# Optimization experiments

Hardware: AMD Instinct MI355X
Metric: run time of the kernel (lower is better)

The kernel has to match this reference:

```python
import jax, jax.numpy as jnp
import numpy as np

B, T, D, FF, H, K = 8, 1024, 512, 2048, 8, 15
HD = D // H  # key_dim = d_model // num_heads


def _ln(x, g, b):
    # keras LayerNormalization default epsilon = 1e-3
    m = jnp.mean(x, axis=-1, keepdims=True)
    v = jnp.var(x, axis=-1, keepdims=True)
    return (x - m) * jax.lax.rsqrt(v + 1e-3) * g + b


def setup_inputs() -> dict:
    key = jax.random.key(0)
    ks = iter(jax.random.split(key, 64))

    def rn(shape, s=0.02):
        return jax.random.normal(next(ks), shape, jnp.float32) * s

    p = {}
    p['x'] = jax.random.normal(next(ks), (B, T, D), jnp.float32)
    # ff_pre: LN -> Dense(FF, relu) -> Dense(D)
    p['g1'] = jnp.ones((D,), jnp.float32); p['b1'] = jnp.zeros((D,), jnp.float32)
    p['Wff1'] = rn((D, FF)); p['bff1'] = jnp.zeros((FF,), jnp.float32)
    p['Wff2'] = rn((FF, D)); p['bff2'] = jnp.zeros((D,), jnp.float32)
    # attention norm + MHA projections (keras EinsumDense shapes)
    p['ga'] = jnp.ones((D,), jnp.float32); p['ba'] = jnp.zeros((D,), jnp.float32)
    p['Wq'] = rn((D, H, HD)); p['bq'] = jnp.zeros((H, HD), jnp.float32)
    p['Wk'] = rn((D, H, HD)); p['bk'] = jnp.zeros((H, HD), jnp.float32)
    p['Wv'] = rn((D, H, HD)); p['bv'] = jnp.zeros((H, HD), jnp.float32)
    p['Wo'] = rn((H, HD, D)); p['bo'] = jnp.zeros((D,), jnp.float32)
    # conv branch: LN -> pointwise conv (2D, gelu) -> depthwise conv(k=15) -> BN -> swish -> pointwise conv (D)
    p['gc'] = jnp.ones((D,), jnp.float32); p['bc'] = jnp.zeros((D,), jnp.float32)
    p['Wcp'] = rn((D, 2 * D)); p['bcp'] = jnp.zeros((2 * D,), jnp.float32)
    p['dwk'] = rn((K, 1, 2 * D)); p['dwb'] = jnp.zeros((2 * D,), jnp.float32)
    p['bn_g'] = jnp.ones((2 * D,), jnp.float32); p['bn_b'] = jnp.zeros((2 * D,), jnp.float32)
    p['bn_m'] = jnp.zeros((2 * D,), jnp.float32)
    p['bn_v'] = jnp.ones((2 * D,), jnp.float32)
    p['Wco'] = rn((2 * D, D)); p['bco'] = jnp.zeros((D,), jnp.float32)
    # ff_post
    p['g2'] = jnp.ones((D,), jnp.float32); p['b2'] = jnp.zeros((D,), jnp.float32)
    p['Wf1'] = rn((D, FF)); p['bf1'] = jnp.zeros((FF,), jnp.float32)
    p['Wf2'] = rn((FF, D)); p['bf2'] = jnp.zeros((D,), jnp.float32)
    return p


def reference(x, g1, b1, Wff1, bff1, Wff2, bff2, ga, ba, Wq, bq, Wk, bk, Wv, bv, Wo, bo, gc, bc, Wcp, bcp, dwk, dwb, bn_g, bn_b, bn_m, bn_v, Wco, bco, g2, b2, Wf1, bf1, Wf2, bf2):
    # Macaron FFN (pre), half-step residual applied later
    x_ff = jnp.maximum(_ln(x, g1, b1) @ Wff1 + bff1, 0.0) @ Wff2 + bff2

    # causal multi-head self-attention (cache=None path)
    a = _ln(x, ga, ba)
    q = jnp.einsum('btd,dhk->bthk', a, Wq) + bq
    k = jnp.einsum('btd,dhk->bthk', a, Wk) + bk
    v = jnp.einsum('btd,dhk->bthk', a, Wv) + bv
    scores = jnp.einsum('bqhd,bkhd->bhqk', q, k) / jnp.sqrt(jnp.float32(HD))
    causal = jnp.tril(jnp.ones((T, T), bool))  # [T,T]
    scores = jnp.where(causal, scores, jnp.float32(-1e9))
    w = jax.nn.softmax(scores, axis=-1)
    ctx = jnp.einsum('bhqk,bkhd->bqhd', w, v)
    attn = jnp.einsum('bqhd,hdo->bqo', ctx, Wo) + bo

    x = x + 0.5 * x_ff + attn

    # convolution module: pointwise(gelu) -> causal left-pad -> depthwise -> BN(inference) -> swish -> pointwise
    c = jax.nn.gelu(_ln(x, gc, bc) @ Wcp + bcp, approximate=False)
    c = jnp.pad(c, ((0, 0), (K - 1, 0), (0, 0)))  # causal pad
    c = jax.lax.conv_general_dilated(
        c, dwk, window_strides=(1,), padding='VALID',
        dimension_numbers=('NWC', 'WIO', 'NWC'), feature_group_count=2 * D) + dwb
    c = (c - bn_m) * jax.lax.rsqrt(bn_v + 1e-3) * bn_g + bn_b
    c = c * jax.nn.sigmoid(c)  # swish
    c = c @ Wco + bco
    x = x + c

    # post FFN (full residual)
    x = x + (jnp.maximum(_ln(x, g2, b2) @ Wf1 + bf1, 0.0) @ Wf2 + bf2)
    return x
```

## Files before the change

### kernel.cpp

```cpp
#include <hip/hip_runtime.h>
#include <hip/hip_bf16.h>
#include <math.h>

#define BB 8
#define TT 1024
#define DD 512
#define FFD 2048
#define HH 8
#define HDD 64
#define KW 15
#define MR (BB*TT)
#define QKVN 1536

typedef __attribute__((ext_vector_type(8))) short short8;
typedef __attribute__((ext_vector_type(4))) short short4v;
typedef __attribute__((ext_vector_type(4))) float f32x4;
typedef __hip_bfloat16 bf16;

__device__ __forceinline__ float bf2f(unsigned u16) {
    return __uint_as_float(u16 << 16);
}

__device__ __forceinline__ void async_copy16(const void* g, void* l) {
    __builtin_amdgcn_global_load_lds(
        (const __attribute__((address_space(1))) void*)g,
        (__attribute__((address_space(3))) void*)l, 16, 0, 0);
}

__device__ __forceinline__ float gelu_exact(float v) {
    return 0.5f * v * (1.0f + erff(v * 0.70710678118654752f));
}

struct PrepPack {
    const float* src[10];
    bf16*        dst[10];
    int          K[10];
    int          lgNT[10];
    float        scale[10];
    int          off[10];
    const float* bq; const float* bk; const float* bv;
    float*       bdst;
    const float* x;
    const float* g1; const float* b1; const float* ga; const float* ba;
    bf16* o1; bf16* o2;
};

__global__ __launch_bounds__(256) void prep_kernel(PrepPack P) {
    __shared__ alignas(16) bf16 T[64][72];
    const int bid = blockIdx.x;
    if (bid == 1536) {
        #pragma unroll
        for (int it = 0; it < 6; ++it) {
            int i = it * 256 + threadIdx.x;
            float v = i < 512 ? P.bq[i] * 0.125f
                              : (i < 1024 ? P.bk[i - 512] : P.bv[i - 1024]);
            P.bdst[i] = v;
        }
        return;
    }
    if (bid > 1536) {
        int wave = ((bid - 1537) * 256 + (int)threadIdx.x) >> 6;
        int lane = threadIdx.x & 63;
        const float* row = P.x + (size_t)wave * DD;
        float4 v0 = ((const float4*)row)[lane];
        float4 v1 = ((const float4*)row)[64 + lane];
        float s  = v0.x + v0.y + v0.z + v0.w + v1.x + v1.y + v1.z + v1.w;
        float ss = v0.x*v0.x + v0.y*v0.y + v0.z*v0.z + v0.w*v0.w
                 + v1.x*v1.x + v1.y*v1.y + v1.z*v1.z + v1.w*v1.w;
        #pragma unroll
        for (int off = 32; off >= 1; off >>= 1) {
            s  += __shfl_xor(s,  off, 64);
            ss += __shfl_xor(ss, off, 64);
        }
        float mean = s * (1.0f / DD);
        float var  = ss * (1.0f / DD) - mean * mean;
        float r    = rsqrtf(var + 1e-3f);
        float n0x = (v0.x - mean) * r, n0y = (v0.y - mean) * r,
              n0z = (v0.z - mean) * r, n0w = (v0.w - mean) * r;
        float n1x = (v1.x - mean) * r, n1y = (v1.y - mean) * r,
              n1z = (v1.z - mean) * r, n1w = (v1.w - mean) * r;
        {
            float4 g0 = ((const float4*)P.g1)[lane];
            float4 gg = ((const float4*)P.g1)[64 + lane];
            float4 b0 = ((const float4*)P.b1)[lane];
            float4 bb = ((const float4*)P.b1)[64 + lane];
            alignas(8) bf16 o0[4], o1[4];
            o0[0] = __float2bfloat16(n0x * g0.x + b0.x);
            o0[1] = __float2bfloat16(n0y * g0.y + b0.y);
            o0[2] = __float2bfloat16(n0z * g0.z + b0.z);
            o0[3] = __float2bfloat16(n0w * g0.w + b0.w);
            o1[0] = __float2bfloat16(n1x * gg.x + bb.x);
            o1[1] = __float2bfloat16(n1y * gg.y + bb.y);
            o1[2] = __float2bfloat16(n1z * gg.z + bb.z);
            o1[3] = __float2bfloat16(n1w * gg.w + bb.w);
            bf16* orow = P.o1 + (size_t)wave * DD;
            *(short4v*)(orow + lane * 4)       = *(const short4v*)o0;
            *(short4v*)(orow + 256 + lane * 4) = *(const short4v*)o1;
        }
        {
            float4 g0 = ((const float4*)P.ga)[lane];
            float4 gg = ((const float4*)P.ga)[64 + lane];
            float4 b0 = ((const float4*)P.ba)[lane];
            float4 bb = ((const float4*)P.ba)[64 + lane];
            alignas(8) bf16 o0[4], o1[4];
            o0[0] = __float2bfloat16(n0x * g0.x + b0.x);
            o0[1] = __float2bfloat16(n0y * g0.y + b0.y);
            o0[2] = __float2bfloat16(n0z * g0.z + b0.z);
            o0[3] = __float2bfloat16(n0w * g0.w + b0.w);
            o1[0] = __float2bfloat16(n1x * gg.x + bb.x);
            o1[1] = __float2bfloat16(n1y * gg.y + bb.y);
            o1[2] = __float2bfloat16(n1z * gg.z + bb.z);
            o1[3] = __float2bfloat16(n1w * gg.w + bb.w);
            bf16* orow = P.o2 + (size_t)wave * DD;
            *(short4v*)(orow + lane * 4)       = *(const short4v*)o0;
            *(short4v*)(orow + 256 + lane * 4) = *(const short4v*)o1;
        }
        return;
    }
    int e = 0;
    #pragma unroll
    for (int i = 1; i < 10; ++i) e = (bid >= P.off[i]) ? i : e;
    const float* W  = P.src[e];
    bf16*        Wt = P.dst[e];
    const int    K  = P.K[e];
    const int    lg = P.lgNT[e];
    const float  scale = P.scale[e];
    const int local = bid - P.off[e];
    const int bx = local & ((1 << lg) - 1);
    const int by = local >> lg;
    const int k0 = by * 64;
    const int n0 = bx * 64;
    const int N  = (1 << lg) * 64;
    const int tid = threadIdx.x;
    #pragma unroll
    for (int it = 0; it < 4; ++it) {
        int lin = it * 256 + tid;
        int kl  = lin >> 4;
        int nq  = (lin & 15) * 4;
        float4 v = *(const float4*)(W + (size_t)(k0 + kl) * N + n0 + nq);
        T[nq + 0][kl] = __float2bfloat16(v.x * scale);
        T[nq + 1][kl] = __float2bfloat16(v.y * scale);
        T[nq + 2][kl] = __float2bfloat16(v.z * scale);
        T[nq + 3][kl] = __float2bfloat16(v.w * scale);
    }
    __syncthreads();
    #pragma unroll
    for (int it = 0; it < 4; ++it) {
        int lin = it * 256 + tid;
        int nl  = lin >> 4;
        int kq  = (lin & 15) * 4;
        *(short4v*)(Wt + (size_t)(n0 + nl) * K + k0 + kq) = *(const short4v*)&T[nl][kq];
    }
}

template<int BN, int OP, int RESMODE, int OUTMODE>
__global__ __launch_bounds__(256) void bgemm_kernel(
    const bf16* __restrict__ A,
    const bf16* __restrict__ Bt,
    const float* __restrict__ bias,
    const float* __restrict__ res1,
    const bf16* __restrict__ res2,
    float s2, float oscale,
    void* __restrict__ Cout,
    int N, int Kd, int nxb)
{
    constexpr int NT = BN / 32;
    constexpr int S  = 4 + BN / 32;
    __shared__ alignas(16) bf16 As[2][128][64];
    __shared__ alignas(16) bf16 Bs[2][BN][64];
    const int tid  = threadIdx.x;
    const int w    = tid >> 6;
    const int lane = tid & 63;
    const int quad = lane >> 4;
    const int l16  = lane & 15;
    const int wm   = w >> 1, wn = w & 1;

    const int flat = blockIdx.x;
    const int c8   = flat & 7;
    const int j    = flat >> 3;
    const int jy   = j / nxb;
    const int m0   = (c8 * 8 + jy) * 128;
    const int n0   = (j - jy * nxb) * BN;

    const int srow = lane >> 3;
    const int scol = ((lane & 7) ^ srow) * 8;

    const bf16* Ap = A  + (size_t)(m0 + w * 32 + srow) * Kd + scol;
    const bf16* Bp = Bt + (size_t)(n0 + w * (BN / 4) + srow) * Kd + scol;

    f32x4 acc[4][NT] = {};
    const int nk = Kd >> 6;

#define BSTAGE(bb, kk) do { \
        _Pragma("unroll") \
        for (int i = 0; i < 4; ++i) \
            async_copy16(Ap + (size_t)(i * 8) * Kd + (kk), &As[bb][w * 32 + i * 8][0]); \
        _Pragma("unroll") \
        for (int i = 0; i < BN / 32; ++i) \
            async_copy16(Bp + (size_t)(i * 8) * Kd + (kk), &Bs[bb][w * (BN / 4) + i * 8][0]); \
    } while (0)

    BSTAGE(0, 0);
    for (int t = 0; t < nk; ++t) {
        const int cur = t & 1;
        if (t + 1 < nk) {
            BSTAGE(cur ^ 1, (t + 1) * 64);
            if constexpr (S == 6) asm volatile("s_waitcnt vmcnt(6)" ::: "memory");
            else                  asm volatile("s_waitcnt vmcnt(8)" ::: "memory");
        } else {
            asm volatile("s_waitcnt vmcnt(0)" ::: "memory");
        }
        __builtin_amdgcn_s_barrier();
        __builtin_amdgcn_sched_barrier(0);
        __builtin_amdgcn_s_setprio(1);
        #pragma unroll
        for (int ks = 0; ks < 2; ++ks) {
            short8 af[4], bfr[NT];
            #pragma unroll
            for (int mt = 0; mt < 4; ++mt) {
                const int row = wm * 64 + mt * 16 + l16;
                const int c   = ((ks * 4 + quad) ^ (row & 7)) * 16;
                af[mt] = *(const short8*)((const char*)&As[cur][row][0] + c);
            }
            #pragma unroll
            for (int nt = 0; nt < NT; ++nt) {
                const int col = wn * (BN / 2) + nt * 16 + l16;
                const int c   = ((ks * 4 + quad) ^ (col & 7)) * 16;
                bfr[nt] = *(const short8*)((const char*)&Bs[cur][col][0] + c);
            }
            #pragma unroll
            for (int mt = 0; mt < 4; ++mt)
                #pragma unroll
                for (int nt = 0; nt < NT; ++nt)
                    acc[mt][nt] = __builtin_amdgcn_mfma_f32_16x16x32_bf16(
                        af[mt], bfr[nt], acc[mt][nt], 0, 0, 0);
        }
        __builtin_amdgcn_s_setprio(0);
        asm volatile("" ::: "memory");
        __builtin_amdgcn_s_barrier();
    }
#undef BSTAGE

    const int crow0 = m0 + wm * 64 + quad * 4;
    const int ccol0 = n0 + wn * (BN / 2) + l16;
    #pragma unroll
    for (int nt = 0; nt < NT; ++nt) {
        const int col = ccol0 + nt * 16;
        const float bv = bias[col];
        #pragma unroll
        for (int mt = 0; mt < 4; ++mt) {
            #pragma unroll
            for (int r = 0; r < 4; ++r) {
                const int row = crow0 + mt * 16 + r;
                const size_t off = (size_t)row * N + col;
                float o = acc[mt][nt][r] + bv;
                if (OP == 1)      o = fmaxf(o, 0.f);
                else if (OP == 2) o = gelu_exact(o);
                if (RESMODE >= 1) o += res1[off];
                if (RESMODE == 2) o += s2 * __bfloat162float(res2[off]);
                if (OUTMODE == 0) ((float*)Cout)[off] = o;
                else              ((bf16*)Cout)[off]  = __float2bfloat16(o * oscale);
            }
        }
    }
}

template<int NK, int RESMODE>
__global__ __launch_bounds__(512, 1) void fusedln_kernel(
    const bf16* __restrict__ A, const bf16* __restrict__ Bt,
    const float* __restrict__ bias,
    const float* __restrict__ res1, const bf16* __restrict__ res2, float s2,
    float* __restrict__ outF,
    const float* __restrict__ g, const float* __restrict__ bb,
    bf16* __restrict__ lnout)
{
    constexpr int Kd = NK * 64;
    __shared__ alignas(16) char lds[2 * 69632];
    const int tid  = threadIdx.x;
    const int w    = tid >> 6;
    const int lane = tid & 63;
    const int quad = lane >> 4;
    const int l16  = lane & 15;
    const int wm   = w >> 2, wn = w & 3;
    const int m0   = (int)blockIdx.x * 32;

    const int srow = lane >> 3;
    const int swz  = ((lane & 7) ^ srow) * 8;
    const bf16* BpS = Bt + (size_t)(w * 64 + srow) * Kd + swz;
    const bf16* ApS = A  + (size_t)(m0 + (w & 3) * 8 + srow) * Kd + swz;

#define FSTG(kc, base) do { \
        _Pragma("unroll") \
        for (int i = 0; i < 8; ++i) \
            async_copy16(BpS + (size_t)(i * 8) * Kd + (kc), \
                         lds + (base) + (w * 64 + i * 8) * 128); \
        if (w < 4) \
            async_copy16(ApS + (kc), \
                         lds + (base) + 65536 + ((w & 3) * 8) * 128); \
    } while (0)

    const int cxa0 = ((quad)     ^ (l16 & 7)) * 16;
    const int cxa1 = ((4 + quad) ^ (l16 & 7)) * 16;

    f32x4 acc[8] = {};

    FSTG(0, 0);
    for (int t = 0; t < NK; ++t) {
        const int cb = (t & 1) * 69632;
        if (t + 1 < NK) {
            FSTG((t + 1) * 64, ((t + 1) & 1) * 69632);
            asm volatile("s_waitcnt vmcnt(8)" ::: "memory");
        } else {
            asm volatile("s_waitcnt vmcnt(0)" ::: "memory");
        }
        __builtin_amdgcn_s_barrier();
        __builtin_amdgcn_sched_barrier(0);
        __builtin_amdgcn_s_setprio(1);

        const char* abase = lds + cb + 65536 + (wm * 16 + l16) * 128;
        short8 a0 = *(const short8*)(abase + cxa0);
        short8 a1 = *(const short8*)(abase + cxa1);
        #pragma unroll
        for (int nt = 0; nt < 8; ++nt) {
            const char* bbase = lds + cb + (wn * 128 + nt * 16 + l16) * 128;
            short8 b0 = *(const short8*)(bbase + cxa0);
            short8 b1 = *(const short8*)(bbase + cxa1);
            acc[nt] = __builtin_amdgcn_mfma_f32_16x16x32_bf16(a0, b0, acc[nt], 0, 0, 0);
            acc[nt] = __builtin_amdgcn_mfma_f32_16x16x32_bf16(a1, b1, acc[nt], 0, 0, 0);
        }
        __builtin_amdgcn_s_setprio(0);
        asm volatile("" ::: "memory");
        __builtin_amdgcn_s_barrier();
    }
#undef FSTG

    const int row0 = m0 + wm * 16 + quad * 4;
    float val[8][4];
    float s[4] = {0.f, 0.f, 0.f, 0.f}, ss[4] = {0.f, 0.f, 0.f, 0.f};
    #pragma unroll
    for (int nt = 0; nt < 8; ++nt) {
        const int col = wn * 128 + nt * 16 + l16;
        const float bv = bias[col];
        #pragma unroll
        for (int r = 0; r < 4; ++r) {
            const size_t off = (size_t)(row0 + r) * DD + col;
            float o = acc[nt][r] + bv;
            if (RESMODE >= 1) o += res1[off];
            if (RESMODE == 2) o += s2 * __bfloat162float(res2[off]);
            outF[off] = o;
            val[nt][r] = o;
            s[r]  += o;
            ss[r] += o * o;
        }
    }
    #pragma unroll
    for (int off = 8; off >= 1; off >>= 1) {
        #pragma unroll
        for (int r = 0; r < 4; ++r) {
            s[r]  += __shfl_xor(s[r],  off, 64);
            ss[r] += __shfl_xor(ss[r], off, 64);
        }
    }
    __syncthreads();
    float2* red = (float2*)lds;
    if (l16 == 0) {
        #pragma unroll
        for (int r = 0; r < 4; ++r) {
            float2 v; v.x = s[r]; v.y = ss[r];
            red[wn * 32 + (wm * 16 + quad * 4 + r)] = v;
        }
    }
    __syncthreads();
    float mean[4], rstd[4];
    #pragma unroll
    for (int r = 0; r < 4; ++r) {
        float a = 0.f, b2 = 0.f;
        #pragma unroll
        for (int q = 0; q < 4; ++q) {
            float2 v = red[q * 32 + (wm * 16 + quad * 4 + r)];
            a += v.x; b2 += v.y;
        }
        const float m = a * (1.0f / DD);
        const float var = b2 * (1.0f / DD) - m * m;
        mean[r] = m;
        rstd[r] = rsqrtf(var + 1e-3f);
    }
    #pragma unroll
    for (int nt = 0; nt < 8; ++nt) {
        const int col = wn * 128 + nt * 16 + l16;
        const float gv = g[col], bv2 = bb[col];
        #pragma unroll
        for (int r = 0; r < 4; ++r) {
            const size_t off = (size_t)(row0 + r) * DD + col;
            lnout[off] = __float2bfloat16(
                (val[nt][r] - mean[r]) * rstd[r] * gv + bv2);
        }
    }
}

__global__ __launch_bounds__(512, 2) void gemm256_kernel(
    const bf16* __restrict__ Aff, const bf16* __restrict__ Btff,
    const float* __restrict__ biasff, bf16* __restrict__ outff,
    const bf16* __restrict__ Aqk, const bf16* __restrict__ Btqk,
    const float* __restrict__ biasqk, bf16* __restrict__ qkvb,
    bf16* __restrict__ Vtb, int nffblk)
{
    __shared__ alignas(16) char lds[131072];
    const int tid  = threadIdx.x;
    const int w    = tid >> 6;
    const int lane = tid & 63;
    const int quad = lane >> 4;
    const int l16  = lane & 15;
    const int ms   = w >> 2, ns = w & 3;

    const bool jobq = (int)blockIdx.x >= nffblk;
    const int  flat = jobq ? (int)blockIdx.x - nffblk : (int)blockIdx.x;
    const int  nxb  = jobq ? 6 : 8;
    const bf16* A   = jobq ? Aqk : Aff;
    const bf16* Bt  = jobq ? Btqk : Btff;
    const float* bias = jobq ? biasqk : biasff;

    const int c8 = flat & 7;
    const int j  = flat >> 3;
    const int jy = j / nxb;
    const int m0 = (c8 * 4 + jy) * 256;
    const int n0 = (j - jy * nxb) * 256;

    const int srow = lane >> 3;
    const int swz  = ((lane & 7) ^ srow) * 8;
    const bf16* ApS = A  + (size_t)(m0 + w * 16 + srow) * DD + swz;
    const bf16* BpS = Bt + (size_t)(n0 + w * 16 + srow) * DD + swz;

#define STG_A(half, kc, nbase) do { \
        async_copy16(ApS + (size_t)((half) * 128) * DD + (kc), \
                     lds + (nbase) + (half) * 16384 + (w * 16) * 128); \
        async_copy16(ApS + (size_t)((half) * 128 + 8) * DD + (kc), \
                     lds + (nbase) + (half) * 16384 + (w * 16 + 8) * 128); \
    } while (0)
#define STG_B(half, kc, nbase) do { \
        async_copy16(BpS + (size_t)((half) * 128) * DD + (kc), \
                     lds + (nbase) + 32768 + (half) * 16384 + (w * 16) * 128); \
        async_copy16(BpS + (size_t)((half) * 128 + 8) * DD + (kc), \
                     lds + (nbase) + 32768 + (half) * 16384 + (w * 16 + 8) * 128); \
    } while (0)

    const int cx0  = ((quad)     ^ (l16 & 7)) * 16;
    const int cx1  = ((4 + quad) ^ (l16 & 7)) * 16;
    const int arow = (ms * 64 + l16) * 128;
    const int brow = (ns * 32 + l16) * 128;

    f32x4 acc[8][4] = {};

    STG_A(0, 0, 0); STG_B(0, 0, 0); STG_B(1, 0, 0); STG_A(1, 0, 0);
    asm volatile("s_waitcnt vmcnt(0)" ::: "memory");

    for (int t = 0; t < 8; ++t) {
        const int cb = (t & 1) * 65536;
        const int nb = cb ^ 65536;

        asm volatile("" ::: "memory");
        __builtin_amdgcn_s_barrier();
        __builtin_amdgcn_sched_barrier(0);

        if (t < 7) {
            const int kn = (t + 1) * 64;
            STG_A(0, kn, nb); STG_B(0, kn, nb);
            STG_B(1, kn, nb); STG_A(1, kn, nb);
        }

        short8 fbv[2][2][2];
        #pragma unroll
        for (int QN = 0; QN < 2; ++QN)
            #pragma unroll
            for (int nt = 0; nt < 2; ++nt) {
                const char* bbase = lds + cb + 32768 + QN * 16384 + brow + nt * 2048;
                fbv[QN][nt][0] = *(const short8*)(bbase + cx0);
                fbv[QN][nt][1] = *(const short8*)(bbase + cx1);
            }
        #pragma unroll
        for (int QM = 0; QM < 2; ++QM) {
            short8 fav[4][2];
            #pragma unroll
            for (int mt = 0; mt < 4; ++mt) {
                const char* abase = lds + cb + QM * 16384 + arow + mt * 2048;
                fav[mt][0] = *(const short8*)(abase + cx0);
                fav[mt][1] = *(const short8*)(abase + cx1);
            }
            #pragma unroll
            for (int QN = 0; QN < 2; ++QN)
                #pragma unroll
                for (int mt = 0; mt < 4; ++mt)
                    #pragma unroll
                    for (int nt = 0; nt < 2; ++nt) {
                        acc[QM * 4 + mt][QN * 2 + nt] =
                            __builtin_amdgcn_mfma_f32_16x16x32_bf16(
                                fav[mt][0], fbv[QN][nt][0],
                                acc[QM * 4 + mt][QN * 2 + nt], 0, 0, 0);
                        acc[QM * 4 + mt][QN * 2 + nt] =
                            __builtin_amdgcn_mfma_f32_16x16x32_bf16(
                                fav[mt][1], fbv[QN][nt][1],
                                acc[QM * 4 + mt][QN * 2 + nt], 0, 0, 0);
                    }
        }

        asm volatile("s_waitcnt vmcnt(0)" ::: "memory");
    }
#undef STG_A
#undef STG_B

    #pragma unroll
    for (int QN = 0; QN < 2; ++QN) {
        #pragma unroll
        for (int nt = 0; nt < 2; ++nt) {
            const int col = n0 + QN * 128 + ns * 32 + nt * 16 + l16;
            const float bv = bias[col];
            #pragma unroll
            for (int QM = 0; QM < 2; ++QM) {
                #pragma unroll
                for (int mt = 0; mt < 4; ++mt) {
                    const f32x4 av = acc[QM * 4 + mt][QN * 2 + nt];
                    const int rowt = m0 + QM * 128 + ms * 64 + mt * 16 + quad * 4;
                    if (jobq) {
                        alignas(8) bf16 o4[4];
                        #pragma unroll
                        for (int r = 0; r < 4; ++r)
                            o4[r] = __float2bfloat16(av[r] + bv);
                        if (col < 1024) {
                            #pragma unroll
                            for (int r = 0; r < 4; ++r)
                                qkvb[(size_t)(rowt + r) * QKVN + col] = o4[r];
                        } else {
                            const int dg  = col - 1024;
                            const int bbk = rowt >> 10, t0 = rowt & 1023;
                            const int bh2 = bbk * 8 + (dg >> 6), d = dg & 63;
                            *(short4v*)(Vtb + ((size_t)bh2 * 64 + d) * TT + t0) =
                                *(const short4v*)o4;
                        }
                    } else {
                        #pragma unroll
                        for (int r = 0; r < 4; ++r) {
                            const float o = fmaxf(av[r] + bv, 0.f);
                            outff[(size_t)(rowt + r) * FFD + col] =
                                __float2bfloat16(o);
                        }
                    }
                }
            }
        }
    }
}

__global__ __launch_bounds__(256) void ff2attn_kernel(
    const bf16* __restrict__ QKV, const bf16* __restrict__ Vt,
    bf16* __restrict__ ctx,
    const bf16* __restrict__ bigb, const bf16* __restrict__ Wff2t,
    const float* __restrict__ bff2, bf16* __restrict__ xffb)
{
    __shared__ alignas(16) bf16 smem[24576];
    const int tid  = threadIdx.x;
    const int w    = tid >> 6;
    const int lane = tid & 63;
    const int quad = lane >> 4;
    const int l16  = lane & 15;
    const int half = (int)blockIdx.x >> 1;

    if ((blockIdx.x & 1) == 0) {
        typedef bf16 (*tile_t)[64][64];
        tile_t Ks = (tile_t)smem;
        tile_t Vs = (tile_t)(smem + 2 * 64 * 64);
        const int bh = half & 63;
        const int bi = 7 - (half >> 6);
        const int b = bh >> 3, h = bh & 7;

        const bf16* Qg = QKV + (size_t)(b * TT) * QKVN + h * 64;
        const bf16* Kg = QKV + (size_t)(b * TT) * QKVN + 512 + h * 64;
        const bf16* Vg = Vt  + (size_t)bh * 64 * TT;

        const int qL = bi * 128 + w * 16;
        const int qH = qL + 64;
        short8 qfL0 = *(const short8*)(Qg + (size_t)(qL + l16) * QKVN + quad * 8);
        short8 qfL1 = *(const short8*)(Qg + (size_t)(qL + l16) * QKVN + 32 + quad * 8);
        short8 qfH0 = *(const short8*)(Qg + (size_t)(qH + l16) * QKVN + quad * 8);
        short8 qfH1 = *(const short8*)(Qg + (size_t)(qH + l16) * QKVN + 32 + quad * 8);

        const int sgrow  = lane >> 3;
        const int sgchnk = lane & 7;

        f32x4 caccL[4] = {}, caccH[4] = {};
        float lL = 0.f, lH = 0.f;
        const int prow_base = ((l16 >> 2) << 3) + (l16 & 3);
        const int smax = 2 * bi + 1;

        #pragma unroll
        for (int i = 0; i < 2; ++i) {
            const int rowbase = w * 8 + i * 32;
            const int row = rowbase + sgrow;
            const int fR = (row & 3) | (((row >> 3) & 1) << 2);
            const int sc = sgchnk ^ fR;
            async_copy16(Kg + (size_t)row * QKVN + sc * 8, &Ks[0][rowbase][0]);
            async_copy16(Vg + (size_t)row * TT + sc * 8,   &Vs[0][rowbase][0]);
        }

        int buf = 0;
        for (int s = 0; s <= smax; ++s) {
            __syncthreads();
            if (s < smax) {
                const int kn = (s + 1) * 64;
                #pragma unroll
                for (int i = 0; i < 2; ++i) {
                    const int rowbase = w * 8 + i * 32;
                    const int row = rowbase + sgrow;
                    const int fR = (row & 3) | (((row >> 3) & 1) << 2);
                    const int sc = sgchnk ^ fR;
                    async_copy16(Kg + (size_t)(kn + row) * QKVN + sc * 8,
                                 &Ks[buf ^ 1][rowbase][0]);
                    async_copy16(Vg + (size_t)row * TT + kn + sc * 8,
                                 &Vs[buf ^ 1][rowbase][0]);
                }
            }
            const int k0 = s * 64;
            const bool doL = (s < smax);

            f32x4 sTL[4], sTH[4];
            __builtin_amdgcn_s_setprio(1);
            #pragma unroll
            for (int s4 = 0; s4 < 4; ++s4) {
                const int prow = prow_base + (s4 >> 1) * 32 + (s4 & 1) * 4;
                const int fR = (prow & 3) | (((prow >> 3) & 1) << 2);
                short8 ka = *(const short8*)&Ks[buf][prow][(quad ^ fR) * 8];
                short8 kb = *(const short8*)&Ks[buf][prow][((4 + quad) ^ fR) * 8];
                f32x4 zH = {0.f, 0.f, 0.f, 0.f};
                zH = __builtin_amdgcn_mfma_f32_16x16x32_bf16(ka, qfH0, zH, 0, 0, 0);
                sTH[s4] = __builtin_amdgcn_mfma_f32_16x16x32_bf16(kb, qfH1, zH, 0, 0, 0);
                if (doL) {
                    f32x4 zL = {0.f, 0.f, 0.f, 0.f};
                    zL = __builtin_amdgcn_mfma_f32_16x16x32_bf16(ka, qfL0, zL, 0, 0, 0);
                    sTL[s4] = __builtin_amdgcn_mfma_f32_16x16x32_bf16(kb, qfL1, zL, 0, 0, 0);
                }
            }
            __builtin_amdgcn_s_setprio(0);

            alignas(16) bf16 pbH[16], pbL[16];
            if (s == smax) {
                const int qg = qH + l16;
                #pragma unroll
                for (int s4 = 0; s4 < 4; ++s4)
                    #pragma unroll
                    for (int r = 0; r < 4; ++r) {
                        const int key = k0 + (s4 >> 1) * 32 + quad * 8 + (s4 & 1) * 4 + r;
                        const float p = (key <= qg) ? __expf(sTH[s4][r]) : 0.f;
                        lH += p;
                        pbH[s4 * 4 + r] = __float2bfloat16(p);
                    }
            } else {
                #pragma unroll
                for (int s4 = 0; s4 < 4; ++s4)
                    #pragma unroll
                    for (int r = 0; r < 4; ++r) {
                        const float p = __expf(sTH[s4][r]);
                        lH += p;
                        pbH[s4 * 4 + r] = __float2bfloat16(p);
                    }
            }
            if (doL) {
                if (s == smax - 1) {
                    const int qg = qL + l16;
                    #pragma unroll
                    for (int s4 = 0; s4 < 4; ++s4)
                        #pragma unroll
                        for (int r = 0; r < 4; ++r) {
                            const int key = k0 + (s4 >> 1) * 32 + quad * 8 + (s4 & 1) * 4 + r;
                            const float p = (key <= qg) ? __expf(sTL[s4][r]) : 0.f;
                            lL += p;
                            pbL[s4 * 4 + r] = __float2bfloat16(p);
                        }
                } else {
                    #pragma unroll
                    for (int s4 = 0; s4 < 4; ++s4)
                        #pragma unroll
                        for (int r = 0; r < 4; ++r) {
                            const float p = __expf(sTL[s4][r]);
                            lL += p;
                            pbL[s4 * 4 + r] = __float2bfloat16(p);
                        }
                }
            }
            const short8 pfH0 = *(const short8*)&pbH[0];
            const short8 pfH1 = *(const short8*)&pbH[8];
            const short8 pfL0 = *(const short8*)&pbL[0];
            const short8 pfL1 = *(const short8*)&pbL[8];

            __builtin_amdgcn_s_setprio(1);
            #pragma unroll
            for (int gg = 0; gg < 4; ++gg) {
                const int vrow = gg * 16 + l16;
                const int fR = (vrow & 3) | (((vrow >> 3) & 1) << 2);
                short8 va = *(const short8*)&Vs[buf][vrow][(quad ^ fR) * 8];
                short8 vb = *(const short8*)&Vs[buf][vrow][((4 + quad) ^ fR) * 8];
                caccH[gg] = __builtin_amdgcn_mfma_f32_16x16x32_bf16(va, pfH0, caccH[gg], 0, 0, 0);
                caccH[gg] = __builtin_amdgcn_mfma_f32_16x16x32_bf16(vb, pfH1, caccH[gg], 0, 0, 0);
                if (doL) {
                    caccL[gg] = __builtin_amdgcn_mfma_f32_16x16x32_bf16(va, pfL0, caccL[gg], 0, 0, 0);
                    caccL[gg] = __builtin_amdgcn_mfma_f32_16x16x32_bf16(vb, pfL1, caccL[gg], 0, 0, 0);
                }
            }
            __builtin_amdgcn_s_setprio(0);
            buf ^= 1;
        }

        lL += __shfl_xor(lL, 16, 64);
        lL += __shfl_xor(lL, 32, 64);
        lH += __shfl_xor(lH, 16, 64);
        lH += __shfl_xor(lH, 32, 64);
        const float invL = 1.0f / lL;
        const float invH = 1.0f / lH;

        bf16* CbL = ctx + (size_t)(b * TT + qL + l16) * DD + h * 64;
        bf16* CbH = ctx + (size_t)(b * TT + qH + l16) * DD + h * 64;
        #pragma unroll
        for (int gg = 0; gg < 4; ++gg) {
            alignas(8) bf16 oL[4], oH[4];
            #pragma unroll
            for (int r = 0; r < 4; ++r) {
                oL[r] = __float2bfloat16(caccL[gg][r] * invL);
                oH[r] = __float2bfloat16(caccH[gg][r] * invH);
            }
            *(short4v*)(CbL + gg * 16 + quad * 4) = *(const short4v*)oL;
            *(short4v*)(CbH + gg * 16 + quad * 4) = *(const short4v*)oH;
        }
    } else {
        const int wm = w >> 1, wn = w & 1;

        const int flat = half;
        const int c8 = flat & 7;
        const int j  = flat >> 3;
        const int jy = j >> 3;
        const int m0 = (c8 * 8 + jy) * 128;
        const int n0 = (j & 7) * 64;

        const int srow = lane >> 3;
        const int scol = ((lane & 7) ^ srow) * 8;

        const bf16* Ap = bigb  + (size_t)(m0 + w * 32 + srow) * FFD + scol;
        const bf16* Bp = Wff2t + (size_t)(n0 + w * 16 + srow) * FFD + scol;

        f32x4 acc[4][2] = {};

#define FSTAGE(bb, kk) do { \
        _Pragma("unroll") \
        for (int i = 0; i < 4; ++i) \
            async_copy16(Ap + (size_t)(i * 8) * FFD + (kk), \
                         smem + (bb) * 8192 + (w * 32 + i * 8) * 64); \
        _Pragma("unroll") \
        for (int i = 0; i < 2; ++i) \
            async_copy16(Bp + (size_t)(i * 8) * FFD + (kk), \
                         smem + 16384 + (bb) * 4096 + (w * 16 + i * 8) * 64); \
    } while (0)

        FSTAGE(0, 0);
        for (int t = 0; t < 32; ++t) {
            const int cur = t & 1;
            if (t < 31) {
                FSTAGE(cur ^ 1, (t + 1) * 64);
                asm volatile("s_waitcnt vmcnt(6)" ::: "memory");
            } else {
                asm volatile("s_waitcnt vmcnt(0)" ::: "memory");
            }
            __builtin_amdgcn_s_barrier();
            __builtin_amdgcn_sched_barrier(0);
            const bf16* AsB = smem + cur * 8192;
            const bf16* BsB = smem + 16384 + cur * 4096;
            __builtin_amdgcn_s_setprio(1);
            #pragma unroll
            for (int ks = 0; ks < 2; ++ks) {
                short8 af[4], bfr[2];
                #pragma unroll
                for (int mt = 0; mt < 4; ++mt) {
                    const int row = wm * 64 + mt * 16 + l16;
                    const int c   = ((ks * 4 + quad) ^ (row & 7)) * 16;
                    af[mt] = *(const short8*)((const char*)(AsB + row * 64) + c);
                }
                #pragma unroll
                for (int nt = 0; nt < 2; ++nt) {
                    const int col = wn * 32 + nt * 16 + l16;
                    const int c   = ((ks * 4 + quad) ^ (col & 7)) * 16;
                    bfr[nt] = *(const short8*)((const char*)(BsB + col * 64) + c);
                }
                #pragma unroll
                for (int mt = 0; mt < 4; ++mt)
                    #pragma unroll
                    for (int nt = 0; nt < 2; ++nt)
                        acc[mt][nt] = __builtin_amdgcn_mfma_f32_16x16x32_bf16(
                            af[mt], bfr[nt], acc[mt][nt], 0, 0, 0);
            }
            __builtin_amdgcn_s_setprio(0);
            asm volatile("" ::: "memory");
            __builtin_amdgcn_s_barrier();
        }
#undef FSTAGE

        const int crow0 = m0 + wm * 64 + quad * 4;
        const int ccol0 = n0 + wn * 32 + l16;
        #pragma unroll
        for (int nt = 0; nt < 2; ++nt) {
            const int col = ccol0 + nt * 16;
            const float bv = bff2[col];
            #pragma unroll
            for (int mt = 0; mt < 4; ++mt)
                #pragma unroll
                for (int r = 0; r < 4; ++r) {
                    const int row = crow0 + mt * 16 + r;
                    xffb[(size_t)row * DD + col] =
                        __float2bfloat16(acc[mt][nt][r] + bv);
                }
        }
    }
}

__global__ __launch_bounds__(256) void dwconv_kernel(const bf16* __restrict__ c1,
                                                     const float* __restrict__ dwk,
                                                     const float* __restrict__ dwb,
                                                     const float* __restrict__ bn_g,
                                                     const float* __restrict__ bn_b,
                                                     const float* __restrict__ bn_m,
                                                     const float* __restrict__ bn_v,
                                                     bf16* __restrict__ out) {
    const int C2 = 2 * DD;
    const int lin = blockIdx.x * 256 + threadIdx.x;
    const int chp = lin & 511;
    const int ch  = chp << 1;
    const int tch = lin >> 9;
    const int row0 = tch << 4;
    const int t0   = row0 & (TT - 1);

    float w0[KW], w1[KW];
    #pragma unroll
    for (int i = 0; i < KW; ++i) {
        w0[i] = dwk[i * C2 + ch];
        w1[i] = dwk[i * C2 + ch + 1];
    }
    const float a0 = rsqrtf(bn_v[ch] + 1e-3f) * bn_g[ch];
    const float a1 = rsqrtf(bn_v[ch + 1] + 1e-3f) * bn_g[ch + 1];
    const float c0 = (dwb[ch] - bn_m[ch]) * a0 + bn_b[ch];
    const float c1v = (dwb[ch + 1] - bn_m[ch + 1]) * a1 + bn_b[ch + 1];

    float x0[30], x1[30];
    if (t0 >= KW - 1) {
        #pragma unroll
        for (int i = 0; i < 30; ++i) {
            unsigned u = *(const unsigned*)(c1 + (size_t)(row0 - (KW - 1) + i) * C2 + ch);
            x0[i] = bf2f(u & 0xffff);
            x1[i] = bf2f(u >> 16);
        }
    } else {
        #pragma unroll
        for (int i = 0; i < 30; ++i) {
            unsigned u = 0;
            if (t0 - (KW - 1) + i >= 0)
                u = *(const unsigned*)(c1 + (size_t)(row0 - (KW - 1) + i) * C2 + ch);
            x0[i] = bf2f(u & 0xffff);
            x1[i] = bf2f(u >> 16);
        }
    }

    #pragma unroll
    for (int j = 0; j < 16; ++j) {
        float s0 = 0.f, s1 = 0.f;
        #pragma unroll
        for (int i = 0; i < KW; ++i) {
            s0 += x0[j + i] * w0[i];
            s1 += x1[j + i] * w1[i];
        }
        s0 = s0 * a0 + c0;
        s1 = s1 * a1 + c1v;
        s0 = s0 / (1.f + __expf(-s0));
        s1 = s1 / (1.f + __expf(-s1));
        alignas(4) bf16 ob[2] = {__float2bfloat16(s0), __float2bfloat16(s1)};
        *(unsigned*)(out + (size_t)(row0 + j) * C2 + ch) = *(const unsigned*)ob;
    }
}

extern "C" void kernel_launch(void* const* d_in, const int* in_sizes, int n_in,
                              void* d_out, int out_size, void* d_ws, size_t ws_size,
                              hipStream_t stream) {
    const float* x    = (const float*)d_in[0];
    const float* g1   = (const float*)d_in[1];
    const float* b1   = (const float*)d_in[2];
    const float* Wff1 = (const float*)d_in[3];
    const float* bff1 = (const float*)d_in[4];
    const float* Wff2 = (const float*)d_in[5];
    const float* bff2 = (const float*)d_in[6];
    const float* ga   = (const float*)d_in[7];
    const float* ba   = (const float*)d_in[8];
    const float* Wq   = (const float*)d_in[9];
    const float* bq   = (const float*)d_in[10];
    const float* Wk   = (const float*)d_in[11];
    const float* bk   = (const float*)d_in[12];
    const float* Wv   = (const float*)d_in[13];
    const float* bv   = (const float*)d_in[14];
    const float* Wo   = (const float*)d_in[15];
    const float* bo   = (const float*)d_in[16];
    const float* gc   = (const float*)d_in[17];
    const float* bc   = (const float*)d_in[18];
    const float* Wcp  = (const float*)d_in[19];
    const float* bcp  = (const float*)d_in[20];
    const float* dwk  = (const float*)d_in[21];
    const float* dwb  = (const float*)d_in[22];
    const float* bn_g = (const float*)d_in[23];
    const float* bn_b = (const float*)d_in[24];
    const float* bn_m = (const float*)d_in[25];
    const float* bn_v = (const float*)d_in[26];
    const float* Wco  = (const float*)d_in[27];
    const float* bco  = (const float*)d_in[28];
    const float* g2   = (const float*)d_in[29];
    const float* b2   = (const float*)d_in[30];
    const float* Wf1  = (const float*)d_in[31];
    const float* bf1  = (const float*)d_in[32];
    const float* Wf2  = (const float*)d_in[33];
    const float* bf2  = (const float*)d_in[34];

    float* out = (float*)d_out;

    char* p = (char*)d_ws;
    bf16* lnb   = (bf16*)p;  p += (size_t)MR * DD * 2;
    bf16* lnab  = (bf16*)p;  p += (size_t)MR * DD * 2;
    bf16* qkvb  = (bf16*)p;  p += (size_t)MR * QKVN * 2;
    bf16* Vtb   = (bf16*)p;  p += (size_t)MR * DD * 2;
    bf16* ctxb  = (bf16*)p;  p += (size_t)MR * DD * 2;
    bf16* xffb  = (bf16*)p;  p += (size_t)MR * DD * 2;
    bf16* bigb  = (bf16*)p;  p += (size_t)MR * FFD * 2;
    bf16* c2b   = (bf16*)p;  p += (size_t)MR * 1024 * 2;
    bf16* Wff1t = (bf16*)p;  p += (size_t)FFD * DD * 2;
    bf16* Wff2t = (bf16*)p;  p += (size_t)DD * FFD * 2;
    bf16* Wqkvt = (bf16*)p;  p += (size_t)QKVN * DD * 2;
    bf16* Wot   = (bf16*)p;  p += (size_t)DD * DD * 2;
    bf16* Wcpt  = (bf16*)p;  p += (size_t)1024 * DD * 2;
    bf16* Wcot  = (bf16*)p;  p += (size_t)DD * 1024 * 2;
    bf16* Wf1t  = (bf16*)p;  p += (size_t)FFD * DD * 2;
    bf16* Wf2t  = (bf16*)p;  p += (size_t)DD * FFD * 2;
    float* bqkv = (float*)p; p += QKVN * 4;

    dim3 blk(256);

    PrepPack P;
    auto set = [&](int i, const float* s, bf16* d, int K, int N, float sc, int off) {
        P.src[i] = s; P.dst[i] = d; P.K[i] = K; P.scale[i] = sc; P.off[i] = off;
        int nt = N / 64, lg = 0; while ((1 << lg) < nt) ++lg; P.lgNT[i] = lg;
    };
    set(0, Wff1, Wff1t, DD,  FFD, 1.f,    0);
    set(1, Wff2, Wff2t, FFD, DD,  1.f,    256);
    set(2, Wq,   Wqkvt,                DD, DD, 0.125f, 512);
    set(3, Wk,   Wqkvt + (size_t)512 * DD,  DD, DD, 1.f, 576);
    set(4, Wv,   Wqkvt + (size_t)1024 * DD, DD, DD, 1.f, 640);
    set(5, Wo,   Wot,   DD,  DD,  1.f,    704);
    set(6, Wcp,  Wcpt,  DD,  1024, 1.f,   768);
    set(7, Wco,  Wcot,  1024, DD, 1.f,    896);
    set(8, Wf1,  Wf1t,  DD,  FFD, 1.f,    1024);
    set(9, Wf2,  Wf2t,  FFD, DD,  1.f,    1280);
    P.bq = bq; P.bk = bk; P.bv = bv; P.bdst = bqkv;
    P.x = x; P.g1 = g1; P.b1 = b1; P.ga = ga; P.ba = ba;
    P.o1 = lnb; P.o2 = lnab;

    prep_kernel<<<dim3(1537 + MR / 4), blk, 0, stream>>>(P);
    gemm256_kernel<<<dim3(448), dim3(512), 0, stream>>>(
        lnb, Wff1t, bff1, bigb, lnab, Wqkvt, bqkv, qkvb, Vtb, 256);
    ff2attn_kernel<<<dim3(1024), blk, 0, stream>>>(
        qkvb, Vtb, ctxb, bigb, Wff2t, bff2, xffb);
    fusedln_kernel<8, 2><<<dim3(256), dim3(512), 0, stream>>>(
        ctxb, Wot, bo, x, xffb, 0.5f, out, gc, bc, lnb);
    bgemm_kernel<128, 2, 0, 1><<<dim3(8 * 64), blk, 0, stream>>>(
        lnb, Wcpt, bcp, nullptr, nullptr, 0.f, 1.f, bigb, 1024, DD, 8);
    dwconv_kernel<<<dim3(MR * 512 / 16 / 256), blk, 0, stream>>>(
        bigb, dwk, dwb, bn_g, bn_b, bn_m, bn_v, c2b);
    fusedln_kernel<16, 1><<<dim3(256), dim3(512), 0, stream>>>(
        c2b, Wcot, bco, out, nullptr, 0.f, out, g2, b2, lnb);
    gemm256_kernel<<<dim3(256), dim3(512), 0, stream>>>(
        lnb, Wf1t, bf1, bigb, nullptr, nullptr, nullptr, nullptr, nullptr, 256);
    bgemm_kernel<64, 0, 1, 0><<<dim3(8 * 64), blk, 0, stream>>>(
        bigb, Wf2t, bf2, out, nullptr, 0.f, 1.f, out, DD, FFD, 8);
}
```

Baseline: 361.5 us.

## Restructure QKV GEMM main loop into four-phase ping-pong pipeline with staggered prefetch

The 256x256 GEMM K-loop is split into four sub-tile phases, each loading its A/B fragments from LDS and then running 16 MFMAs. Global-to-LDS async copies for the next two K-steps are staggered across the phases, and a partial vmcnt wait replaces the full drain at the end of each iteration. s_setprio is raised around the MFMA phases so waves alternate between memory and compute. The goal is to overlap global loads with compute and shorten barrier stalls, at the cost of more barriers per iteration and fragile hand-counted vmcnt and buffer reuse ordering.

```diff
diff --git a/kernel.cpp b/kernel.cpp
--- a/kernel.cpp
+++ b/kernel.cpp
@@ -450,61 +450,94 @@
     const int brow = (ns * 32 + l16) * 128;
 
     f32x4 acc[8][4] = {};
+    short8 aq[4][2], b0q[2][2], b1q[2][2];
+
+#define MFMA16(QM, QN, BQ) \
+    _Pragma("unroll") \
+    for (int mt = 0; mt < 4; ++mt) \
+        _Pragma("unroll") \
+        for (int nt = 0; nt < 2; ++nt) { \
+            acc[(QM) * 4 + mt][(QN) * 2 + nt] = \
+                __builtin_amdgcn_mfma_f32_16x16x32_bf16( \
+                    aq[mt][0], BQ[nt][0], acc[(QM) * 4 + mt][(QN) * 2 + nt], 0, 0, 0); \
+            acc[(QM) * 4 + mt][(QN) * 2 + nt] = \
+                __builtin_amdgcn_mfma_f32_16x16x32_bf16( \
+                    aq[mt][1], BQ[nt][1], acc[(QM) * 4 + mt][(QN) * 2 + nt], 0, 0, 0); \
+        }
+
+#define PH_SYNC \
+    __builtin_amdgcn_s_barrier(); \
+    asm volatile("s_waitcnt lgkmcnt(0)" ::: "memory"); \
+    __builtin_amdgcn_sched_barrier(0); \
+    __builtin_amdgcn_s_setprio(1);
+
+#define PH_END \
+    __builtin_amdgcn_s_setprio(0); \
+    asm volatile("" ::: "memory"); \
+    __builtin_amdgcn_s_barrier();
 
     STG_A(0, 0, 0); STG_B(0, 0, 0); STG_B(1, 0, 0); STG_A(1, 0, 0);
-    asm volatile("s_waitcnt vmcnt(0)" ::: "memory");
+    STG_A(0, 64, 65536); STG_B(0, 64, 65536); STG_B(1, 64, 65536);
+    asm volatile("s_waitcnt vmcnt(6)" ::: "memory");
+    __builtin_amdgcn_s_barrier();
 
     for (int t = 0; t < 8; ++t) {
         const int cb = (t & 1) * 65536;
         const int nb = cb ^ 65536;
-
-        asm volatile("" ::: "memory");
+        const int kn1 = (t + 1) * 64;
+        const int kn2 = (t + 2) * 64;
+
+        #pragma unroll
+        for (int mt = 0; mt < 4; ++mt) {
+            const char* ab = lds + cb + arow + mt * 2048;
+            aq[mt][0] = *(const short8*)(ab + cx0);
+            aq[mt][1] = *(const short8*)(ab + cx1);
+        }
+        #pragma unroll
+        for (int nt = 0; nt < 2; ++nt) {
+            const char* bbp = lds + cb + 32768 + brow + nt * 2048;
+            b0q[nt][0] = *(const short8*)(bbp + cx0);
+            b0q[nt][1] = *(const short8*)(bbp + cx1);
+        }
+        if (t < 7) STG_A(1, kn1, nb);
+        PH_SYNC
+        MFMA16(0, 0, b0q)
+        PH_END
+
+        #pragma unroll
+        for (int nt = 0; nt < 2; ++nt) {
+            const char* bbp = lds + cb + 49152 + brow + nt * 2048;
+            b1q[nt][0] = *(const short8*)(bbp + cx0);
+            b1q[nt][1] = *(const short8*)(bbp + cx1);
+        }
+        if (t < 6) STG_A(0, kn2, cb);
+        PH_SYNC
+        MFMA16(0, 1, b1q)
+        PH_END
+
+        #pragma unroll
+        for (int mt = 0; mt < 4; ++mt) {
+            const char* ab = lds + cb + 16384 + arow + mt * 2048;
+            aq[mt][0] = *(const short8*)(ab + cx0);
+            aq[mt][1] = *(const short8*)(ab + cx1);
+        }
+        if (t < 6) STG_B(0, kn2, cb);
+        PH_SYNC
+        MFMA16(1, 0, b0q)
+        PH_END
+
+        if (t < 6) STG_B(1, kn2, cb);
+        if (t < 6)       { asm volatile("s_waitcnt vmcnt(6)" ::: "memory"); }
+        else if (t == 6) { asm volatile("s_waitcnt vmcnt(0)" ::: "memory"); }
         __builtin_amdgcn_s_barrier();
         __builtin_amdgcn_sched_barrier(0);
-
-        if (t < 7) {
-            const int kn = (t + 1) * 64;
-            STG_A(0, kn, nb); STG_B(0, kn, nb);
-            STG_B(1, kn, nb); STG_A(1, kn, nb);
-        }
-
-        short8 fbv[2][2][2];
-        #pragma unroll
-        for (int QN = 0; QN < 2; ++QN)
-            #pragma unroll
-            for (int nt = 0; nt < 2; ++nt) {
-                const char* bbase = lds + cb + 32768 + QN * 16384 + brow + nt * 2048;
-                fbv[QN][nt][0] = *(const short8*)(bbase + cx0);
-                fbv[QN][nt][1] = *(const short8*)(bbase + cx1);
-            }
-        #pragma unroll
-        for (int QM = 0; QM < 2; ++QM) {
-            short8 fav[4][2];
-            #pragma unroll
-            for (int mt = 0; mt < 4; ++mt) {
-                const char* abase = lds + cb + QM * 16384 + arow + mt * 2048;
-                fav[mt][0] = *(const short8*)(abase + cx0);
-                fav[mt][1] = *(const short8*)(abase + cx1);
-            }
-            #pragma unroll
-            for (int QN = 0; QN < 2; ++QN)
-                #pragma unroll
-                for (int mt = 0; mt < 4; ++mt)
-                    #pragma unroll
-                    for (int nt = 0; nt < 2; ++nt) {
-                        acc[QM * 4 + mt][QN * 2 + nt] =
-                            __builtin_amdgcn_mfma_f32_16x16x32_bf16(
-                                fav[mt][0], fbv[QN][nt][0],
-                                acc[QM * 4 + mt][QN * 2 + nt], 0, 0, 0);
-                        acc[QM * 4 + mt][QN * 2 + nt] =
-                            __builtin_amdgcn_mfma_f32_16x16x32_bf16(
-                                fav[mt][1], fbv[QN][nt][1],
-                                acc[QM * 4 + mt][QN * 2 + nt], 0, 0, 0);
-                    }
-        }
-
-        asm volatile("s_waitcnt vmcnt(0)" ::: "memory");
-    }
+        __builtin_amdgcn_s_setprio(1);
+        MFMA16(1, 1, b1q)
+        PH_END
+    }
+#undef PH_SYNC
+#undef PH_END
+#undef MFMA16
 #undef STG_A
 #undef STG_B
 
```

After: 363.5 us. No clear change (+0.5%).

## Defer later-layer weight transposes into the attention kernel's tail blocks

Applied to the files above, without the earlier changes.

The prep kernel now transposes and converts only the weights needed by the first GEMM and attention (FF1, FF2, QKV). The remaining five weight transposes (Wo, Wcp, Wco, Wf1, Wf2) run as 832 extra blocks appended to the ff2attn launch. The aim is to take them off the critical path at startup and let them fill idle compute units while the causal-attention blocks run. The risk is that these extra blocks compete for resources with the attention work or lengthen the tail of that launch.

```diff
diff --git a/kernel.cpp b/kernel.cpp
--- a/kernel.cpp
+++ b/kernel.cpp
@@ -32,12 +32,12 @@
 }
 
 struct PrepPack {
-    const float* src[10];
-    bf16*        dst[10];
-    int          K[10];
-    int          lgNT[10];
-    float        scale[10];
-    int          off[10];
+    const float* src[5];
+    bf16*        dst[5];
+    int          K[5];
+    int          lgNT[5];
+    float        scale[5];
+    int          off[5];
     const float* bq; const float* bk; const float* bv;
     float*       bdst;
     const float* x;
@@ -45,10 +45,47 @@
     bf16* o1; bf16* o2;
 };
 
+__device__ __forceinline__ void transpose_tile(const PrepPack& P, int bid,
+                                               bf16 (*T)[72], int tid) {
+    int e = 0;
+    #pragma unroll
+    for (int i = 1; i < 5; ++i) e = (bid >= P.off[i]) ? i : e;
+    const float* W  = P.src[e];
+    bf16*        Wt = P.dst[e];
+    const int    K  = P.K[e];
+    const int    lg = P.lgNT[e];
+    const float  scale = P.scale[e];
+    const int local = bid - P.off[e];
+    const int bx = local & ((1 << lg) - 1);
+    const int by = local >> lg;
+    const int k0 = by * 64;
+    const int n0 = bx * 64;
+    const int N  = (1 << lg) * 64;
+    #pragma unroll
+    for (int it = 0; it < 4; ++it) {
+        int lin = it * 256 + tid;
+        int kl  = lin >> 4;
+        int nq  = (lin & 15) * 4;
+        float4 v = *(const float4*)(W + (size_t)(k0 + kl) * N + n0 + nq);
+        T[nq + 0][kl] = __float2bfloat16(v.x * scale);
+        T[nq + 1][kl] = __float2bfloat16(v.y * scale);
+        T[nq + 2][kl] = __float2bfloat16(v.z * scale);
+        T[nq + 3][kl] = __float2bfloat16(v.w * scale);
+    }
+    __syncthreads();
+    #pragma unroll
+    for (int it = 0; it < 4; ++it) {
+        int lin = it * 256 + tid;
+        int nl  = lin >> 4;
+        int kq  = (lin & 15) * 4;
+        *(short4v*)(Wt + (size_t)(n0 + nl) * K + k0 + kq) = *(const short4v*)&T[nl][kq];
+    }
+}
+
 __global__ __launch_bounds__(256) void prep_kernel(PrepPack P) {
     __shared__ alignas(16) bf16 T[64][72];
     const int bid = blockIdx.x;
-    if (bid == 1536) {
+    if (bid == 704) {
         #pragma unroll
         for (int it = 0; it < 6; ++it) {
             int i = it * 256 + threadIdx.x;
@@ -58,8 +95,8 @@
         }
         return;
     }
-    if (bid > 1536) {
-        int wave = ((bid - 1537) * 256 + (int)threadIdx.x) >> 6;
+    if (bid > 704) {
+        int wave = ((bid - 705) * 256 + (int)threadIdx.x) >> 6;
         int lane = threadIdx.x & 63;
         const float* row = P.x + (size_t)wave * DD;
         float4 v0 = ((const float4*)row)[lane];
@@ -117,40 +154,7 @@
         }
         return;
     }
-    int e = 0;
-    #pragma unroll
-    for (int i = 1; i < 10; ++i) e = (bid >= P.off[i]) ? i : e;
-    const float* W  = P.src[e];
-    bf16*        Wt = P.dst[e];
-    const int    K  = P.K[e];
-    const int    lg = P.lgNT[e];
-    const float  scale = P.scale[e];
-    const int local = bid - P.off[e];
-    const int bx = local & ((1 << lg) - 1);
-    const int by = local >> lg;
-    const int k0 = by * 64;
-    const int n0 = bx * 64;
-    const int N  = (1 << lg) * 64;
-    const int tid = threadIdx.x;
-    #pragma unroll
-    for (int it = 0; it < 4; ++it) {
-        int lin = it * 256 + tid;
-        int kl  = lin >> 4;
-        int nq  = (lin & 15) * 4;
-        float4 v = *(const float4*)(W + (size_t)(k0 + kl) * N + n0 + nq);
-        T[nq + 0][kl] = __float2bfloat16(v.x * scale);
-        T[nq + 1][kl] = __float2bfloat16(v.y * scale);
-        T[nq + 2][kl] = __float2bfloat16(v.z * scale);
-        T[nq + 3][kl] = __float2bfloat16(v.w * scale);
-    }
-    __syncthreads();
-    #pragma unroll
-    for (int it = 0; it < 4; ++it) {
-        int lin = it * 256 + tid;
-        int nl  = lin >> 4;
-        int kq  = (lin & 15) * 4;
-        *(short4v*)(Wt + (size_t)(n0 + nl) * K + k0 + kq) = *(const short4v*)&T[nl][kq];
-    }
+    transpose_tile(P, bid, T, threadIdx.x);
 }
 
 template<int BN, int OP, int RESMODE, int OUTMODE>
@@ -554,7 +558,8 @@
     const bf16* __restrict__ QKV, const bf16* __restrict__ Vt,
     bf16* __restrict__ ctx,
     const bf16* __restrict__ bigb, const bf16* __restrict__ Wff2t,
-    const float* __restrict__ bff2, bf16* __restrict__ xffb)
+    const float* __restrict__ bff2, bf16* __restrict__ xffb,
+    PrepPack P2)
 {
     __shared__ alignas(16) bf16 smem[24576];
     const int tid  = threadIdx.x;
@@ -562,6 +567,12 @@
     const int lane = tid & 63;
     const int quad = lane >> 4;
     const int l16  = lane & 15;
+
+    if ((int)blockIdx.x >= 1024) {
+        typedef bf16 (*tp72)[72];
+        transpose_tile(P2, (int)blockIdx.x - 1024, (tp72)smem, tid);
+        return;
+    }
     const int half = (int)blockIdx.x >> 1;
 
     if ((blockIdx.x & 1) == 0) {
@@ -942,30 +953,37 @@
 
     dim3 blk(256);
 
-    PrepPack P;
-    auto set = [&](int i, const float* s, bf16* d, int K, int N, float sc, int off) {
+    auto fill = [](PrepPack& P, int i, const float* s, bf16* d, int K, int N,
+                   float sc, int off) {
         P.src[i] = s; P.dst[i] = d; P.K[i] = K; P.scale[i] = sc; P.off[i] = off;
         int nt = N / 64, lg = 0; while ((1 << lg) < nt) ++lg; P.lgNT[i] = lg;
     };
-    set(0, Wff1, Wff1t, DD,  FFD, 1.f,    0);
-    set(1, Wff2, Wff2t, FFD, DD,  1.f,    256);
-    set(2, Wq,   Wqkvt,                DD, DD, 0.125f, 512);
-    set(3, Wk,   Wqkvt + (size_t)512 * DD,  DD, DD, 1.f, 576);
-    set(4, Wv,   Wqkvt + (size_t)1024 * DD, DD, DD, 1.f, 640);
-    set(5, Wo,   Wot,   DD,  DD,  1.f,    704);
-    set(6, Wcp,  Wcpt,  DD,  1024, 1.f,   768);
-    set(7, Wco,  Wcot,  1024, DD, 1.f,    896);
-    set(8, Wf1,  Wf1t,  DD,  FFD, 1.f,    1024);
-    set(9, Wf2,  Wf2t,  FFD, DD,  1.f,    1280);
+
+    PrepPack P;
+    fill(P, 0, Wff1, Wff1t, DD,  FFD, 1.f,    0);
+    fill(P, 1, Wff2, Wff2t, FFD, DD,  1.f,    256);
+    fill(P, 2, Wq,   Wqkvt,                 DD, DD, 0.125f, 512);
+    fill(P, 3, Wk,   Wqkvt + (size_t)512 * DD,  DD, DD, 1.f, 576);
+    fill(P, 4, Wv,   Wqkvt + (size_t)1024 * DD, DD, DD, 1.f, 640);
     P.bq = bq; P.bk = bk; P.bv = bv; P.bdst = bqkv;
     P.x = x; P.g1 = g1; P.b1 = b1; P.ga = ga; P.ba = ba;
     P.o1 = lnb; P.o2 = lnab;
 
-    prep_kernel<<<dim3(1537 + MR / 4), blk, 0, stream>>>(P);
+    PrepPack P2;
+    fill(P2, 0, Wo,  Wot,  DD,   DD,   1.f, 0);
+    fill(P2, 1, Wcp, Wcpt, DD,   1024, 1.f, 64);
+    fill(P2, 2, Wco, Wcot, 1024, DD,   1.f, 192);
+    fill(P2, 3, Wf1, Wf1t, DD,   FFD,  1.f, 320);
+    fill(P2, 4, Wf2, Wf2t, FFD,  DD,   1.f, 576);
+    P2.bq = bq; P2.bk = bk; P2.bv = bv; P2.bdst = bqkv;
+    P2.x = x; P2.g1 = g1; P2.b1 = b1; P2.ga = ga; P2.ba = ba;
+    P2.o1 = lnb; P2.o2 = lnab;
+
+    prep_kernel<<<dim3(705 + MR / 4), blk, 0, stream>>>(P);
     gemm256_kernel<<<dim3(448), dim3(512), 0, stream>>>(
         lnb, Wff1t, bff1, bigb, lnab, Wqkvt, bqkv, qkvb, Vtb, 256);
-    ff2attn_kernel<<<dim3(1024), blk, 0, stream>>>(
-        qkvb, Vtb, ctxb, bigb, Wff2t, bff2, xffb);
+    ff2attn_kernel<<<dim3(1856), blk, 0, stream>>>(
+        qkvb, Vtb, ctxb, bigb, Wff2t, bff2, xffb, P2);
     fusedln_kernel<8, 2><<<dim3(256), dim3(512), 0, stream>>>(
         ctxb, Wot, bo, x, xffb, 0.5f, out, gc, bc, lnb);
     bgemm_kernel<128, 2, 0, 1><<<dim3(8 * 64), blk, 0, stream>>>(
```

After: 362.9 us. No clear change (+0.4%).
